# Optimization experiments

Measured on AMD Instinct MI355X. Metric: run time of the kernel, lower is better.

## Reference

```python
import jax, jax.numpy as jnp
import numpy as np

OBJ_N, D_KEY, D_VAL, BANK_N, N_Q, BS = 4, 128, 512, 7200, 3600, 1


def setup_inputs() -> dict:
    key = jax.random.key(0)
    k1, k2, k3, k4, k5 = jax.random.split(key, 5)
    return {
        "keys": jax.random.normal(k1, (OBJ_N, D_KEY, BANK_N), dtype=jnp.float32),
        "values": jax.random.normal(k2, (OBJ_N, D_VAL, BANK_N), dtype=jnp.float32),
        "masks": jax.random.uniform(k3, (OBJ_N, 1, BANK_N), dtype=jnp.float32),
        "q_in": jax.random.normal(k4, (BS, D_KEY, N_Q), dtype=jnp.float32),
        "q_out": jax.random.normal(k5, (BS, D_VAL, N_Q), dtype=jnp.float32),
    }


def reference(keys, values, masks, q_in, q_out):
    # keys: (O, Dk, B) memory keys per object; q_in: (S, Dk, N) query keys
    d_key = keys.shape[1]
    scale = 1.0 / jnp.sqrt(jnp.asarray(d_key, dtype=keys.dtype))
    # p[o,s,b,n] = softmax_b( keys[o,:,b] . q_in[s,:,n] / sqrt(Dk) )
    logits = jnp.einsum('odb,sdn->osbn', keys, q_in) * scale
    p = jax.nn.softmax(logits, axis=2)
    # mem[o,s,v,n] = sum_b values[o,v,b] * p[o,s,b,n]
    mem = jnp.einsum('ovb,osbn->osvn', values, p)
    # mask_mem[o,s,1,n]: mask-weighted attention readout, gates q_out
    mask_mem = jnp.einsum('omb,osbn->osmn', masks, p)
    q_out_with_mask = q_out[None] * mask_mem          # (O, S, Dv, N)
    out = jnp.concatenate([mem, q_out_with_mask], axis=2)  # (O, S, 2*Dv, N)
    return jnp.transpose(out, (1, 0, 2, 3))           # (S, O, 2*Dv, N)
```

## Files before the change

kernel.cpp:

```cpp
#include <hip/hip_runtime.h>
#include <hip/hip_bf16.h>

typedef unsigned short u16;
typedef unsigned int   u32;
typedef short bf16x8 __attribute__((ext_vector_type(8)));
typedef float f32x4  __attribute__((ext_vector_type(4)));

#define O_N    4
#define D_K    128
#define D_V    512
#define BANK   7200
#define NQ     3600
#define NT     64
#define BT     32
#define NTILES 57
#define ITERS  (BANK/BT)
#define VH_ROWS 256

#define K_OFF    0
#define P_OFF    16384
#define LMM_OFF  20480
#define SMEM_BYTES 20992
#define Q_OFF    0

#define GLL(gsrc, ldst) __builtin_amdgcn_global_load_lds( \
    (const __attribute__((address_space(1))) void*)(gsrc), \
    (__attribute__((address_space(3))) void*)(ldst), 16, 0, 0)

static __device__ __forceinline__ u16 f2bf(float x) {
    u32 u = __builtin_bit_cast(u32, x);
    return (u16)((u + 0x7FFFu + ((u >> 16) & 1u)) >> 16);
}


__global__ void k_transpose_bf16(const float* __restrict__ in, u16* __restrict__ out) {
    __shared__ float tile[32][33];
    const int obj = blockIdx.z;
    const float* src = in + (size_t)obj * D_K * BANK;
    u16* dst = out + (size_t)obj * BANK * D_K;
    const int bx = blockIdx.x * 32;
    const int by = blockIdx.y * 32;
    const int tx = threadIdx.x, ty = threadIdx.y;
#pragma unroll
    for (int i = 0; i < 4; i++)
        tile[ty + 8 * i][tx] = src[(size_t)(by + ty + 8 * i) * BANK + bx + tx];
    __syncthreads();
#pragma unroll
    for (int i = 0; i < 4; i++)
        dst[(size_t)(bx + ty + 8 * i) * D_K + by + tx] = f2bf(tile[tx][ty + 8 * i]);
}

__global__ void k_convert_bf16(const float* __restrict__ in, u16* __restrict__ out, int n4) {
    int idx = blockIdx.x * blockDim.x + threadIdx.x;
    int stride = gridDim.x * blockDim.x;
    for (int i = idx; i < n4; i += stride) {
        float4 v = reinterpret_cast<const float4*>(in)[i];
        ushort4 o;
        o.x = f2bf(v.x); o.y = f2bf(v.y); o.z = f2bf(v.z); o.w = f2bf(v.w);
        reinterpret_cast<ushort4*>(out)[i] = o;
    }
}

__global__ void k_zero(float* out, int n) {
    int i = blockIdx.x * blockDim.x + threadIdx.x;
    if (i < n) out[i] = 0.f;
}

__launch_bounds__(256, 3)
__global__ void k_matcher(const u16* __restrict__ Kt,
                          const u16* __restrict__ Vb,
                          const float* __restrict__ masks,
                          const float* __restrict__ q_in,
                          const float* __restrict__ q_out,
                          float* __restrict__ out,
                          int G, float* __restrict__ lw, float* __restrict__ mw)
{
    __shared__ __align__(16) char smem[SMEM_BYTES];
    const int tid  = threadIdx.x;
    const int wave = tid >> 6;
    const int lane = tid & 63;
    const int q    = lane >> 4;
    const int lr   = lane & 15;

    const int grp  = blockIdx.x & 7;
    const int o    = grp >> 1;
    const int vh   = grp & 1;
    const int rest = blockIdx.x >> 3;
    const int tile = rest / G;
    const int g    = rest - tile * G;
    const int n0   = tile * NT;
    const int it0  = (ITERS * g) / G;
    const int it1  = (ITERS * (g + 1)) / G;
    const int nit  = it1 - it0;

    for (int idx = tid; idx < NT * D_K; idx += 256) {
        int d = idx >> 6;
        int n = idx & 63;
        int gn = n0 + n;
        float v = (gn < NQ) ? q_in[(size_t)d * NQ + gn] : 0.f;
        int bb = d * 2;
        int sb = n * 256 + ((((bb >> 4) ^ (n & 7)) << 4) | (bb & 15));
        *reinterpret_cast<u16*>(smem + Q_OFF + sb) = f2bf(v);
    }
    __syncthreads();

    bf16x8 qf[4];
    {
        const int n = 16 * wave + lr;
#pragma unroll
        for (int ds = 0; ds < 4; ds++) {
            int gq = (4 * ds + q) ^ (n & 7);
            qf[ds] = *reinterpret_cast<const bf16x8*>(smem + Q_OFF + n * 256 + gq * 16);
        }
    }
    __syncthreads();

    const f32x4 zero4 = {0.f, 0.f, 0.f, 0.f};
    f32x4 acc[4][4];
#pragma unroll
    for (int i = 0; i < 4; i++)
#pragma unroll
        for (int j = 0; j < 4; j++) acc[i][j] = zero4;
    float l_part = 0.f, mm_part = 0.f;
    const float scale = 0.08838834764831845f;

    const u16* Ko = Kt + (size_t)o * BANK * D_K;
    const u16* Vo = Vb + (size_t)o * D_V * BANK + (size_t)vh * VH_ROWS * BANK;
    const float* mPtr = masks + (size_t)o * BANK + it0 * BT + 4 * q;

    const u16* kSrcA = Ko + (size_t)(it0 * BT + (tid >> 4)) * D_K
                         + (((tid & 15) ^ ((tid >> 4) & 7)) << 3);
    const u16* kSrcB = Ko + (size_t)(it0 * BT + ((tid + 256) >> 4)) * D_K
                         + ((((tid + 256) & 15) ^ (((tid + 256) >> 4) & 7)) << 3);

#define ISSUE_K(buf) do {                                                  \
        char* kb_ = smem + K_OFF + (buf) * 8192 + wave * 1024;             \
        GLL(kSrcA, kb_);                                                   \
        GLL(kSrcB, kb_ + 4096);                                            \
        kSrcA += BT * D_K; kSrcB += BT * D_K;                              \
    } while (0)

    const u16* Vrow = Vo + it0 * BT;
    const u32  vOff = (u32)(64 * wave + lr) * BANK + q * 8;

    ISSUE_K(0);

    for (int ii = 0; ii < nit; ii++) {
        const int cur = ii & 1;
        asm volatile("s_waitcnt vmcnt(0)" ::: "memory");
        __builtin_amdgcn_s_barrier();
        __builtin_amdgcn_sched_barrier(0);

        float4 mv0 = *reinterpret_cast<const float4*>(mPtr);
        float4 mv1 = *reinterpret_cast<const float4*>(mPtr + 16);
        bf16x8 vf0 = *reinterpret_cast<const bf16x8*>(Vrow + vOff);
        bf16x8 vf1 = *reinterpret_cast<const bf16x8*>(Vrow + vOff + 16 * BANK);
        bf16x8 vf2 = *reinterpret_cast<const bf16x8*>(Vrow + vOff + 32 * BANK);
        bf16x8 vf3 = *reinterpret_cast<const bf16x8*>(Vrow + vOff + 48 * BANK);
        if (ii + 1 < nit) ISSUE_K(cur ^ 1);
        mPtr += BT;
        Vrow += BT;

        const char* kb = smem + K_OFF + cur * 8192;
#pragma unroll
        for (int t = 0; t < 2; t++) {
            f32x4 s_acc = zero4;
            const int b_r = 16 * t + lr;
#pragma unroll
            for (int ds = 0; ds < 4; ds++) {
                int gk = (4 * ds + q) ^ (lr & 7);
                bf16x8 kf = *reinterpret_cast<const bf16x8*>(kb + b_r * 256 + gk * 16);
                s_acc = __builtin_amdgcn_mfma_f32_16x16x32_bf16(kf, qf[ds], s_acc, 0, 0, 0);
            }
            const float4 mv = t ? mv1 : mv0;
            float p0 = __expf(s_acc[0] * scale);
            float p1 = __expf(s_acc[1] * scale);
            float p2 = __expf(s_acc[2] * scale);
            float p3 = __expf(s_acc[3] * scale);
            l_part  += p0 + p1 + p2 + p3;
            mm_part += p0 * mv.x + p1 * mv.y + p2 * mv.z + p3 * mv.w;
            ushort4 pk;
            pk.x = f2bf(p0); pk.y = f2bf(p1); pk.z = f2bf(p2); pk.w = f2bf(p3);
            const int n = 16 * wave + lr;
            int gp = (2 * t + (q >> 1)) ^ (n & 3);
            *reinterpret_cast<ushort4*>(smem + P_OFF + n * 64 + gp * 16 + (q & 1) * 8) = pk;
        }

        asm volatile("s_waitcnt lgkmcnt(0)" ::: "memory");
        __builtin_amdgcn_s_barrier();
        __builtin_amdgcn_sched_barrier(0);

#pragma unroll
        for (int ng = 0; ng < 4; ng++) {
            int n = 16 * ng + lr;
            bf16x8 pf = *reinterpret_cast<const bf16x8*>(
                smem + P_OFF + n * 64 + ((q ^ (n & 3)) << 4));
            acc[0][ng] = __builtin_amdgcn_mfma_f32_16x16x32_bf16(vf0, pf, acc[0][ng], 0, 0, 0);
            acc[1][ng] = __builtin_amdgcn_mfma_f32_16x16x32_bf16(vf1, pf, acc[1][ng], 0, 0, 0);
            acc[2][ng] = __builtin_amdgcn_mfma_f32_16x16x32_bf16(vf2, pf, acc[2][ng], 0, 0, 0);
            acc[3][ng] = __builtin_amdgcn_mfma_f32_16x16x32_bf16(vf3, pf, acc[3][ng], 0, 0, 0);
        }
    }

    l_part  += __shfl_xor(l_part, 16);  l_part  += __shfl_xor(l_part, 32);
    mm_part += __shfl_xor(mm_part, 16); mm_part += __shfl_xor(mm_part, 32);
    float* l_lds  = reinterpret_cast<float*>(smem + LMM_OFF);
    float* mm_lds = l_lds + 64;
    if (lane < 16) {
        l_lds[16 * wave + lr]  = l_part;
        mm_lds[16 * wave + lr] = mm_part;
    }
    __syncthreads();

    if (G == 1) {
        float* outo = out + (size_t)o * (1024 * NQ);
#pragma unroll
        for (int ng = 0; ng < 4; ng++) {
            const int n  = 16 * ng + lr;
            const int gn = n0 + n;
            if (gn >= NQ) continue;
            const float invl = 1.f / l_lds[n];
            const float gate = mm_lds[n] * invl;
#pragma unroll
            for (int vt = 0; vt < 4; vt++) {
#pragma unroll
                for (int r = 0; r < 4; r++) {
                    const int v = vh * VH_ROWS + 64 * wave + 16 * vt + 4 * q + r;
                    outo[(size_t)v * NQ + gn] = acc[vt][ng][r] * invl;
                    outo[(size_t)(512 + v) * NQ + gn] = q_out[(size_t)v * NQ + gn] * gate;
                }
            }
        }
    } else {
        float* dst = out + ((size_t)o * 1024 + (size_t)g * 512 + (size_t)vh * VH_ROWS) * NQ;
#pragma unroll
        for (int ng = 0; ng < 4; ng++) {
            const int n  = 16 * ng + lr;
            const int gn = n0 + n;
            if (gn >= NQ) continue;
#pragma unroll
            for (int vt = 0; vt < 4; vt++) {
#pragma unroll
                for (int r = 0; r < 4; r++) {
                    const int v = 64 * wave + 16 * vt + 4 * q + r;
                    dst[(size_t)v * NQ + gn] = acc[vt][ng][r];
                }
            }
        }
        if (vh == 0 && tid < 64) {
            const size_t li = ((size_t)(g * 4 + o) * NTILES + tile) * 64 + tid;
            lw[li] = l_lds[tid];
            mw[li] = mm_lds[tid];
        }
    }
}

__global__ void k_combine(const float* __restrict__ q_out, const float* __restrict__ lw,
                          const float* __restrict__ mw, float* __restrict__ out) {
    const int total = O_N * 512 * (NQ / 4);
    float4* outv = reinterpret_cast<float4*>(out);
    const float4* qv = reinterpret_cast<const float4*>(q_out);
    for (int idx = blockIdx.x * blockDim.x + threadIdx.x; idx < total;
         idx += gridDim.x * blockDim.x) {
        const int o  = idx / (512 * 900);
        const int r  = idx - o * 512 * 900;
        const int v  = r / 900;
        const int g4 = r - v * 900;
        const size_t iA = ((size_t)o * 1024 + v) * 900 + g4;
        const size_t iB = ((size_t)o * 1024 + 512 + v) * 900 + g4;
        float4 A = outv[iA];
        float4 B = outv[iB];
        const int tl = g4 >> 4;
        const int wi = (g4 & 15) * 4;
        const size_t l0i = ((size_t)(0 * 4 + o) * NTILES + tl) * 64 + wi;
        const size_t l1i = ((size_t)(1 * 4 + o) * NTILES + tl) * 64 + wi;
        const float4 l0 = *reinterpret_cast<const float4*>(lw + l0i);
        const float4 l1 = *reinterpret_cast<const float4*>(lw + l1i);
        const float4 m0 = *reinterpret_cast<const float4*>(mw + l0i);
        const float4 m1 = *reinterpret_cast<const float4*>(mw + l1i);
        float4 li, mem, gate;
        li.x = 1.f / (l0.x + l1.x); li.y = 1.f / (l0.y + l1.y);
        li.z = 1.f / (l0.z + l1.z); li.w = 1.f / (l0.w + l1.w);
        mem.x = (A.x + B.x) * li.x; mem.y = (A.y + B.y) * li.y;
        mem.z = (A.z + B.z) * li.z; mem.w = (A.w + B.w) * li.w;
        gate.x = (m0.x + m1.x) * li.x; gate.y = (m0.y + m1.y) * li.y;
        gate.z = (m0.z + m1.z) * li.z; gate.w = (m0.w + m1.w) * li.w;
        float4 qo = qv[(size_t)v * 900 + g4];
        outv[iA] = mem;
        float4 gq;
        gq.x = qo.x * gate.x; gq.y = qo.y * gate.y;
        gq.z = qo.z * gate.z; gq.w = qo.w * gate.w;
        outv[iB] = gq;
    }
}

extern "C" void kernel_launch(void* const* d_in, const int* in_sizes, int n_in,
                              void* d_out, int out_size, void* d_ws, size_t ws_size,
                              hipStream_t stream) {
    const float* keys   = (const float*)d_in[0];
    const float* values = (const float*)d_in[1];
    const float* masks  = (const float*)d_in[2];
    const float* q_in   = (const float*)d_in[3];
    const float* q_outp = (const float*)d_in[4];
    float* out = (float*)d_out;

    const size_t K_BYTES  = (size_t)O_N * BANK * D_K * 2;
    const size_t V_BYTES  = (size_t)O_N * D_V * BANK * 2;
    const size_t LM_FLOATS = (size_t)2 * O_N * NTILES * 64;
    const size_t LM_BYTES  = LM_FLOATS * 4 * 2;

    if (ws_size < K_BYTES + V_BYTES) {
        k_zero<<<(out_size + 255) / 256, 256, 0, stream>>>(out, out_size);
        return;
    }
    const int G = (ws_size >= K_BYTES + V_BYTES + LM_BYTES) ? 2 : 1;

    u16* Kt = (u16*)d_ws;
    u16* Vb = (u16*)((char*)d_ws + K_BYTES);
    float* lw = (float*)((char*)d_ws + K_BYTES + V_BYTES);
    float* mw = lw + LM_FLOATS;

    dim3 tb(32, 8);
    dim3 tg(BANK / 32, D_K / 32, O_N);
    k_transpose_bf16<<<tg, tb, 0, stream>>>(keys, Kt);

    const int n4 = O_N * D_V * BANK / 4;
    k_convert_bf16<<<2048, 256, 0, stream>>>(values, Vb, n4);

    k_matcher<<<NTILES * 8 * G, 256, 0, stream>>>(Kt, Vb, masks, q_in, q_outp, out,
                                                  G, lw, mw);
    if (G == 2)
        k_combine<<<2048, 256, 0, stream>>>(q_outp, lw, mw, out);
}
```

Before: 336.1 us.

## Process two 32-row bank subtiles per pipeline step to halve barriers

```diff
diff --git a/kernel.cpp b/kernel.cpp
--- a/kernel.cpp
+++ b/kernel.cpp
@@ -12,20 +12,21 @@
 #define BANK   7200
 #define NQ     3600
 #define NT     64
-#define BT     32
 #define NTILES 57
-#define ITERS  (BANK/BT)
+#define NSUB   225
 #define VH_ROWS 256
 
 #define K_OFF    0
-#define P_OFF    16384
-#define LMM_OFF  20480
-#define SMEM_BYTES 20992
+#define P_OFF    32768
+#define LMM_OFF  40960
+#define SMEM_BYTES 41472
 #define Q_OFF    0
 
 #define GLL(gsrc, ldst) __builtin_amdgcn_global_load_lds( \
     (const __attribute__((address_space(1))) void*)(gsrc), \
     (__attribute__((address_space(3))) void*)(ldst), 16, 0, 0)
+
+#define MFMA16(a, b, c) __builtin_amdgcn_mfma_f32_16x16x32_bf16((a), (b), (c), 0, 0, 0)
 
 static __device__ __forceinline__ u16 f2bf(float x) {
     u32 u = __builtin_bit_cast(u32, x);
@@ -81,6 +82,7 @@
     const int lane = tid & 63;
     const int q    = lane >> 4;
     const int lr   = lane & 15;
+    const int lr7  = lr & 7;
 
     const int grp  = blockIdx.x & 7;
     const int o    = grp >> 1;
@@ -89,9 +91,13 @@
     const int tile = rest / G;
     const int g    = rest - tile * G;
     const int n0   = tile * NT;
-    const int it0  = (ITERS * g) / G;
-    const int it1  = (ITERS * (g + 1)) / G;
-    const int nit  = it1 - it0;
+
+    const int st0 = (NSUB * g) / G;
+    const int st1 = (NSUB * (g + 1)) / G;
+    const int cnt = st1 - st0;
+    const int nd  = cnt >> 1;
+    const int ts  = cnt & 1;
+    const int nu  = nd + ts;
 
     for (int idx = tid; idx < NT * D_K; idx += 256) {
         int d = idx >> 6;
@@ -126,79 +132,112 @@
 
     const u16* Ko = Kt + (size_t)o * BANK * D_K;
     const u16* Vo = Vb + (size_t)o * D_V * BANK + (size_t)vh * VH_ROWS * BANK;
-    const float* mPtr = masks + (size_t)o * BANK + it0 * BT + 4 * q;
-
-    const u16* kSrcA = Ko + (size_t)(it0 * BT + (tid >> 4)) * D_K
+    const float* mPtr = masks + (size_t)o * BANK + st0 * 32 + 4 * q;
+
+    const u16* kSrcA = Ko + (size_t)(st0 * 32 + (tid >> 4)) * D_K
                          + (((tid & 15) ^ ((tid >> 4) & 7)) << 3);
-    const u16* kSrcB = Ko + (size_t)(it0 * BT + ((tid + 256) >> 4)) * D_K
-                         + ((((tid + 256) & 15) ^ (((tid + 256) >> 4) & 7)) << 3);
-
-#define ISSUE_K(buf) do {                                                  \
-        char* kb_ = smem + K_OFF + (buf) * 8192 + wave * 1024;             \
+    const u16* kSrcB = kSrcA + 16 * D_K;
+
+#define ISSUE2(buf) do {                                                   \
+        char* kb_ = smem + K_OFF + (buf) * 16384 + wave * 1024;            \
         GLL(kSrcA, kb_);                                                   \
         GLL(kSrcB, kb_ + 4096);                                            \
-        kSrcA += BT * D_K; kSrcB += BT * D_K;                              \
+        GLL(kSrcA + 32 * D_K, kb_ + 8192);                                 \
+        GLL(kSrcB + 32 * D_K, kb_ + 12288);                                \
+        kSrcA += 64 * D_K; kSrcB += 64 * D_K;                              \
     } while (0)
-
-    const u16* Vrow = Vo + it0 * BT;
+#define ISSUE1(buf) do {                                                   \
+        char* kb_ = smem + K_OFF + (buf) * 16384 + wave * 1024;            \
+        GLL(kSrcA, kb_);                                                   \
+        GLL(kSrcB, kb_ + 4096);                                            \
+    } while (0)
+
+    const u16* Vrow = Vo + st0 * 32;
     const u32  vOff = (u32)(64 * wave + lr) * BANK + q * 8;
 
-    ISSUE_K(0);
-
-    for (int ii = 0; ii < nit; ii++) {
-        const int cur = ii & 1;
+    const int nrow  = 16 * wave + lr;
+    char* const pW  = smem + P_OFF + nrow * 128 + (q & 1) * 8;
+
+#define QK_T(T, MV) do {                                                     \
+        f32x4 s_acc = zero4;                                                 \
+        const int b_r = 16 * (T) + lr;                                       \
+        _Pragma("unroll")                                                    \
+        for (int ds = 0; ds < 4; ds++) {                                     \
+            bf16x8 kf = *reinterpret_cast<const bf16x8*>(                    \
+                kb + b_r * 256 + (((4 * ds + q) ^ lr7) << 4));               \
+            s_acc = MFMA16(kf, qf[ds], s_acc);                               \
+        }                                                                    \
+        float p0 = __expf(s_acc[0] * scale);                                 \
+        float p1 = __expf(s_acc[1] * scale);                                 \
+        float p2 = __expf(s_acc[2] * scale);                                 \
+        float p3 = __expf(s_acc[3] * scale);                                 \
+        l_part  += p0 + p1 + p2 + p3;                                        \
+        mm_part += p0 * (MV).x + p1 * (MV).y + p2 * (MV).z + p3 * (MV).w;    \
+        ushort4 pk;                                                          \
+        pk.x = f2bf(p0); pk.y = f2bf(p1); pk.z = f2bf(p2); pk.w = f2bf(p3);  \
+        *reinterpret_cast<ushort4*>(                                         \
+            pW + (((2 * (T) + (q >> 1)) ^ lr7) << 4)) = pk;                  \
+    } while (0)
+
+#define PV_S(S, V0, V1, V2, V3) do {                                         \
+        _Pragma("unroll")                                                    \
+        for (int ng = 0; ng < 4; ng++) {                                     \
+            bf16x8 pf = *reinterpret_cast<const bf16x8*>(                    \
+                smem + P_OFF + (16 * ng + lr) * 128 +                        \
+                (((4 * (S) + q) ^ lr7) << 4));                               \
+            acc[0][ng] = MFMA16(V0, pf, acc[0][ng]);                         \
+            acc[1][ng] = MFMA16(V1, pf, acc[1][ng]);                         \
+            acc[2][ng] = MFMA16(V2, pf, acc[2][ng]);                         \
+            acc[3][ng] = MFMA16(V3, pf, acc[3][ng]);                         \
+        }                                                                    \
+    } while (0)
+
+    if (nd > 0) ISSUE2(0); else ISSUE1(0);
+
+    for (int u = 0; u < nu; u++) {
+        const int cur = u & 1;
         asm volatile("s_waitcnt vmcnt(0)" ::: "memory");
         __builtin_amdgcn_s_barrier();
         __builtin_amdgcn_sched_barrier(0);
-
-        float4 mv0 = *reinterpret_cast<const float4*>(mPtr);
-        float4 mv1 = *reinterpret_cast<const float4*>(mPtr + 16);
-        bf16x8 vf0 = *reinterpret_cast<const bf16x8*>(Vrow + vOff);
-        bf16x8 vf1 = *reinterpret_cast<const bf16x8*>(Vrow + vOff + 16 * BANK);
-        bf16x8 vf2 = *reinterpret_cast<const bf16x8*>(Vrow + vOff + 32 * BANK);
-        bf16x8 vf3 = *reinterpret_cast<const bf16x8*>(Vrow + vOff + 48 * BANK);
-        if (ii + 1 < nit) ISSUE_K(cur ^ 1);
-        mPtr += BT;
-        Vrow += BT;
-
-        const char* kb = smem + K_OFF + cur * 8192;
-#pragma unroll
-        for (int t = 0; t < 2; t++) {
-            f32x4 s_acc = zero4;
-            const int b_r = 16 * t + lr;
-#pragma unroll
-            for (int ds = 0; ds < 4; ds++) {
-                int gk = (4 * ds + q) ^ (lr & 7);
-                bf16x8 kf = *reinterpret_cast<const bf16x8*>(kb + b_r * 256 + gk * 16);
-                s_acc = __builtin_amdgcn_mfma_f32_16x16x32_bf16(kf, qf[ds], s_acc, 0, 0, 0);
-            }
-            const float4 mv = t ? mv1 : mv0;
-            float p0 = __expf(s_acc[0] * scale);
-            float p1 = __expf(s_acc[1] * scale);
-            float p2 = __expf(s_acc[2] * scale);
-            float p3 = __expf(s_acc[3] * scale);
-            l_part  += p0 + p1 + p2 + p3;
-            mm_part += p0 * mv.x + p1 * mv.y + p2 * mv.z + p3 * mv.w;
-            ushort4 pk;
-            pk.x = f2bf(p0); pk.y = f2bf(p1); pk.z = f2bf(p2); pk.w = f2bf(p3);
-            const int n = 16 * wave + lr;
-            int gp = (2 * t + (q >> 1)) ^ (n & 3);
-            *reinterpret_cast<ushort4*>(smem + P_OFF + n * 64 + gp * 16 + (q & 1) * 8) = pk;
-        }
-
-        asm volatile("s_waitcnt lgkmcnt(0)" ::: "memory");
-        __builtin_amdgcn_s_barrier();
-        __builtin_amdgcn_sched_barrier(0);
-
-#pragma unroll
-        for (int ng = 0; ng < 4; ng++) {
-            int n = 16 * ng + lr;
-            bf16x8 pf = *reinterpret_cast<const bf16x8*>(
-                smem + P_OFF + n * 64 + ((q ^ (n & 3)) << 4));
-            acc[0][ng] = __builtin_amdgcn_mfma_f32_16x16x32_bf16(vf0, pf, acc[0][ng], 0, 0, 0);
-            acc[1][ng] = __builtin_amdgcn_mfma_f32_16x16x32_bf16(vf1, pf, acc[1][ng], 0, 0, 0);
-            acc[2][ng] = __builtin_amdgcn_mfma_f32_16x16x32_bf16(vf2, pf, acc[2][ng], 0, 0, 0);
-            acc[3][ng] = __builtin_amdgcn_mfma_f32_16x16x32_bf16(vf3, pf, acc[3][ng], 0, 0, 0);
+        if (u + 1 < nu) {
+            if (u + 1 < nd) ISSUE2(cur ^ 1);
+            else            ISSUE1(cur ^ 1);
+        }
+        const char* kb = smem + K_OFF + cur * 16384;
+
+        if (u < nd) {
+            float4 mv0 = *reinterpret_cast<const float4*>(mPtr);
+            float4 mv1 = *reinterpret_cast<const float4*>(mPtr + 16);
+            float4 mv2 = *reinterpret_cast<const float4*>(mPtr + 32);
+            float4 mv3 = *reinterpret_cast<const float4*>(mPtr + 48);
+            bf16x8 va0 = *reinterpret_cast<const bf16x8*>(Vrow + vOff);
+            bf16x8 va1 = *reinterpret_cast<const bf16x8*>(Vrow + vOff + 16 * BANK);
+            bf16x8 va2 = *reinterpret_cast<const bf16x8*>(Vrow + vOff + 32 * BANK);
+            bf16x8 va3 = *reinterpret_cast<const bf16x8*>(Vrow + vOff + 48 * BANK);
+            QK_T(0, mv0); QK_T(1, mv1); QK_T(2, mv2); QK_T(3, mv3);
+            bf16x8 vb0 = *reinterpret_cast<const bf16x8*>(Vrow + vOff + 32);
+            bf16x8 vb1 = *reinterpret_cast<const bf16x8*>(Vrow + vOff + 32 + 16 * BANK);
+            bf16x8 vb2 = *reinterpret_cast<const bf16x8*>(Vrow + vOff + 32 + 32 * BANK);
+            bf16x8 vb3 = *reinterpret_cast<const bf16x8*>(Vrow + vOff + 32 + 48 * BANK);
+            asm volatile("s_waitcnt lgkmcnt(0)" ::: "memory");
+            __builtin_amdgcn_s_barrier();
+            __builtin_amdgcn_sched_barrier(0);
+            PV_S(0, va0, va1, va2, va3);
+            PV_S(1, vb0, vb1, vb2, vb3);
+            mPtr += 64;
+            Vrow += 64;
+        } else {
+            float4 mv0 = *reinterpret_cast<const float4*>(mPtr);
+            float4 mv1 = *reinterpret_cast<const float4*>(mPtr + 16);
+            bf16x8 va0 = *reinterpret_cast<const bf16x8*>(Vrow + vOff);
+            bf16x8 va1 = *reinterpret_cast<const bf16x8*>(Vrow + vOff + 16 * BANK);
+            bf16x8 va2 = *reinterpret_cast<const bf16x8*>(Vrow + vOff + 32 * BANK);
+            bf16x8 va3 = *reinterpret_cast<const bf16x8*>(Vrow + vOff + 48 * BANK);
+            QK_T(0, mv0); QK_T(1, mv1);
+            asm volatile("s_waitcnt lgkmcnt(0)" ::: "memory");
+            __builtin_amdgcn_s_barrier();
+            __builtin_amdgcn_sched_barrier(0);
+            PV_S(0, va0, va1, va2, va3);
         }
     }
 
```

After: 853.5 us. 154% more time.
